# Optimization experiments

Measured on AMD Instinct MI355X. Metric: run time of the kernel, lower is better.

Reference implementation:

```python
import jax, jax.numpy as jnp
import numpy as np

V = 32000   # vocab_size
H = 256     # num_hiddens
B = 32      # batch
T = 128     # seq_len


def setup_inputs() -> dict:
    key = jax.random.key(0)
    ks = jax.random.split(key, 10)
    s = 0.05  # keep pre-activations in a sane range
    return {
        "X": jax.random.randint(ks[0], (B, T), 0, V),
        "H0": jnp.zeros((B, H), jnp.float32),
        "Wz": (jax.random.normal(ks[1], (H, V + H)) * s).astype(jnp.float32),
        "bz": (jax.random.normal(ks[2], (H,)) * s).astype(jnp.float32),
        "Wr": (jax.random.normal(ks[3], (H, V + H)) * s).astype(jnp.float32),
        "br": (jax.random.normal(ks[4], (H,)) * s).astype(jnp.float32),
        "Wh": (jax.random.normal(ks[5], (H, V + H)) * s).astype(jnp.float32),
        "bh": (jax.random.normal(ks[6], (H,)) * s).astype(jnp.float32),
        "Wo": (jax.random.normal(ks[7], (V, H)) * s).astype(jnp.float32),
        "bo": (jax.random.normal(ks[8], (V,)) * s).astype(jnp.float32),
    }


def reference(X, H0, Wz, bz, Wr, br, Wh, bh, Wo, bo):
    # nn.Linear(cat(one_hot(x), h)) == gather of the vocab-columns + h @ Wh.T.
    # one_hot(x) @ W[:, :V].T  ==  W[:, :V].T[x]  (row gather), same math, no dense one-hot GEMM.
    vocab = Wo.shape[0]
    Wz_x, Wz_h = Wz[:, :vocab], Wz[:, vocab:]
    Wr_x, Wr_h = Wr[:, :vocab], Wr[:, vocab:]
    Wh_x, Wh_h = Wh[:, :vocab], Wh[:, vocab:]

    Xt = X.T                 # [T, B] -- matches X.T in torch forward
    gz = Wz_x.T[Xt]          # [T, B, H]
    gr = Wr_x.T[Xt]          # [T, B, H]
    gh = Wh_x.T[Xt]          # [T, B, H]

    def step(Hs, g):
        gz_t, gr_t, gh_t = g
        z = jax.nn.sigmoid(gz_t + Hs @ Wz_h.T + bz)
        r = jax.nn.sigmoid(gr_t + Hs @ Wr_h.T + br)
        h = jnp.tanh(gh_t + (r * Hs) @ Wh_h.T + bh)
        Hn = z * h + (1.0 - z) * Hs
        Y = Hn @ Wo.T + bo   # [B, V]
        return Hn, Y

    Hf, Ys = jax.lax.scan(step, H0, (gz, gr, gh))  # Ys: [T, B, V]
    # torch.cat(outputs, dim=0) stacks time-major -> [T*B, V]
    return Ys.reshape(-1, vocab), Hf
```

## Files before the change

### kernel.cpp

```cpp
#include <hip/hip_runtime.h>
#include <hip/hip_fp16.h>
#include <stdint.h>

#define VV 32000
#define HH 256
#define BB 32
#define TT 128
#define VH 32256

typedef _Float16 f16;
typedef _Float16 f16x2 __attribute__((ext_vector_type(2)));
typedef _Float16 f16x8 __attribute__((ext_vector_type(8)));
typedef float f32x4 __attribute__((ext_vector_type(4)));

static __device__ __forceinline__ float dot2f(uint32_t w, uint32_t h, float acc){
  f16x2 a = __builtin_bit_cast(f16x2, w);
  f16x2 b = __builtin_bit_cast(f16x2, h);
#if __has_builtin(__builtin_amdgcn_fdot2)
  return __builtin_amdgcn_fdot2(a, b, acc, false);
#else
  acc = fmaf((float)a[0], (float)b[0], acc);
  acc = fmaf((float)a[1], (float)b[1], acc);
  return acc;
#endif
}

__global__ void k_gather(const int* __restrict__ X,
                         const float* __restrict__ Wz, const float* __restrict__ bz,
                         const float* __restrict__ Wr, const float* __restrict__ br,
                         const float* __restrict__ Wh, const float* __restrict__ bh,
                         float* __restrict__ g_buf){
  int tb = blockIdx.x;
  int t = tb >> 5, b = tb & 31;
  int tok = X[b*TT + t];
  int o = threadIdx.x;
  g_buf[(size_t)tb*768 + o]       = Wz[(size_t)o*VH + tok] + bz[o];
  g_buf[(size_t)tb*768 + 256 + o] = Wr[(size_t)o*VH + tok] + br[o];
  g_buf[(size_t)tb*768 + 512 + o] = Wh[(size_t)o*VH + tok] + bh[o];
}

__global__ void k_pack(const float* __restrict__ Wz, const float* __restrict__ Wr,
                       const float* __restrict__ Wh, uint32_t* __restrict__ Wpack){
  int idx = blockIdx.x*256 + threadIdx.x;
  if (idx >= 512*192) return;
  int t = idx / 192, rem = idx - t*192;
  int ol = rem >> 4, p = rem & 15;
  int ko = t & 7, no = t >> 3;
  int k = ko*32 + p*2;
  const float* W; int row;
  if (ol < 8){ int o = no*8 + ol; if (o < 256){ W = Wz; row = o; } else { W = Wr; row = o - 256; } }
  else { W = Wh; row = no*4 + (ol - 8); }
  float a = W[(size_t)row*VH + VV + k];
  float c = W[(size_t)row*VH + VV + k + 1];
  f16x2 v; v[0] = (f16)a; v[1] = (f16)c;
  Wpack[idx] = __builtin_bit_cast(uint32_t, v);
}

__global__ __launch_bounds__(512)
__attribute__((amdgpu_waves_per_eu(2, 2)))
void k_recur(const float* __restrict__ H0,
             const uint32_t* __restrict__ Wpack,
             const float* __restrict__ g_buf,
             f16* __restrict__ Hn16,
             float* __restrict__ hf_out){
  __shared__ __align__(16) uint32_t hs16[128];
  __shared__ __align__(16) f16 rHs16[256];
  __shared__ float hs32[256];
  __shared__ float z_s[256];

  const int b = blockIdx.x;
  const int tid = threadIdx.x;
  const int ko = tid & 7, no = tid >> 3;

  uint32_t w[12][16];
  {
    const uint4* src = (const uint4*)(Wpack + (size_t)tid*192);
    #pragma unroll
    for (int j=0;j<48;j++){
      uint4 v = src[j];
      int f = j*4;
      w[(f+0)>>4][(f+0)&15] = v.x;
      w[(f+1)>>4][(f+1)&15] = v.y;
      w[(f+2)>>4][(f+2)&15] = v.z;
      w[(f+3)>>4][(f+3)&15] = v.w;
    }
  }

  if (tid < 256) hs32[tid] = H0[b*HH + tid];
  __syncthreads();
  if (tid < 128){
    f16x2 v; v[0] = (f16)hs32[2*tid]; v[1] = (f16)hs32[2*tid+1];
    hs16[tid] = __builtin_bit_cast(uint32_t, v);
  }
  __syncthreads();

  const int gi1 = no*8 + ko;
  const int gi2 = 512 + no*4 + (ko & 3);
  float g1 = g_buf[(size_t)b*768 + gi1];
  float g2 = g_buf[(size_t)b*768 + gi2];
  float g1n = 0.f, g2n = 0.f;

  for (int t = 0; t < TT; t++){
    if (t < TT-1){
      const float* gn = g_buf + (size_t)((t+1)*BB + b)*768;
      g1n = gn[gi1];
      g2n = gn[gi2];
    }

    uint32_t hp[16];
    {
      const uint2* hsp = (const uint2*)hs16;
      #pragma unroll
      for (int j=0;j<8;j++){ uint2 v = hsp[ko*8 + j]; hp[2*j] = v.x; hp[2*j+1] = v.y; }
    }
    float acc[8];
    #pragma unroll
    for (int ol=0;ol<8;ol++) acc[ol] = 0.f;
    #pragma unroll
    for (int p=0;p<16;p++)
      #pragma unroll
      for (int ol=0;ol<8;ol++)
        acc[ol] = dot2f(w[ol][p], hp[p], acc[ol]);
    #pragma unroll
    for (int ol=0;ol<8;ol++){
      float v2 = acc[ol];
      v2 += __shfl_xor(v2, 1);
      v2 += __shfl_xor(v2, 2);
      v2 += __shfl_xor(v2, 4);
      acc[ol] = v2;
    }
    {
      float sel = acc[0];
      #pragma unroll
      for (int ol=1;ol<8;ol++) sel = (ko == ol) ? acc[ol] : sel;
      float pre = sel + g1;
      float s = 1.f / (1.f + __expf(-pre));
      int o = no*8 + ko;
      if (no < 32){
        z_s[o] = s;
      } else {
        int op = o - 256;
        rHs16[op] = (f16)(s * hs32[op]);
      }
    }
    __syncthreads();

    uint32_t rp[16];
    {
      const uint2* rpp = (const uint2*)rHs16;
      #pragma unroll
      for (int j=0;j<8;j++){ uint2 v = rpp[ko*8 + j]; rp[2*j] = v.x; rp[2*j+1] = v.y; }
    }
    float a2[4];
    #pragma unroll
    for (int oi=0;oi<4;oi++) a2[oi] = 0.f;
    #pragma unroll
    for (int p=0;p<16;p++)
      #pragma unroll
      for (int oi=0;oi<4;oi++)
        a2[oi] = dot2f(w[8+oi][p], rp[p], a2[oi]);
    #pragma unroll
    for (int oi=0;oi<4;oi++){
      float v2 = a2[oi];
      v2 += __shfl_xor(v2, 1);
      v2 += __shfl_xor(v2, 2);
      v2 += __shfl_xor(v2, 4);
      a2[oi] = v2;
    }
    if (ko < 4){
      float sel = a2[0];
      #pragma unroll
      for (int oi=1;oi<4;oi++) sel = (ko == oi) ? a2[oi] : sel;
      int o = no*4 + ko;
      float pre = sel + g2;
      float ax = fabsf(pre);
      float e = __expf(2.f*ax);
      float th = 1.f - 2.f/(e + 1.f);
      th = copysignf(th, pre);
      float z = z_s[o];
      float hn = z*th + (1.f - z)*hs32[o];
      hs32[o] = hn;
      ((f16*)hs16)[o] = (f16)hn;
      Hn16[(size_t)(t*BB + b)*HH + o] = (f16)hn;
      if (t == TT-1) hf_out[b*HH + o] = hn;
    }
    g1 = g1n; g2 = g2n;
    __syncthreads();
  }
}

__global__ __launch_bounds__(256) void k_gemm(const f16* __restrict__ A, const float* __restrict__ Wo,
                                              const float* __restrict__ bo, float* __restrict__ Y){
  __shared__ __align__(16) f16 a_lds[128*128];
  __shared__ __align__(16) f16 b_lds[128*128];
  const int m0 = blockIdx.x * 128;
  const int n0 = blockIdx.y * 128;
  const int tid = threadIdx.x;
  const int lane = tid & 63, wave = tid >> 6;
  const int wm = wave >> 1, wn = wave & 1;

  f32x4 acc[4][4];
  {
    f32x4 z = {0.f, 0.f, 0.f, 0.f};
    #pragma unroll
    for (int i=0;i<4;i++)
      #pragma unroll
      for (int j=0;j<4;j++) acc[i][j] = z;
  }

  const int srow = tid >> 1, seg = tid & 1;
  #pragma unroll 1
  for (int kt=0; kt<2; kt++){
    const int k0 = kt*128;
    {
      const uint4* asrc = (const uint4*)(A + (size_t)(m0+srow)*256 + k0 + seg*64);
      #pragma unroll
      for (int j=0;j<8;j++){
        uint4 v = asrc[j];
        int byte = (srow*256 + seg*128 + j*16) ^ ((srow&7)<<4);
        *(uint4*)((char*)a_lds + byte) = v;
      }
      const float4* bsrc = (const float4*)(Wo + (size_t)(n0+srow)*256 + k0 + seg*64);
      #pragma unroll
      for (int j=0;j<8;j++){
        float4 f0 = bsrc[2*j], f1 = bsrc[2*j+1];
        f16x8 hv;
        hv[0]=(f16)f0.x; hv[1]=(f16)f0.y; hv[2]=(f16)f0.z; hv[3]=(f16)f0.w;
        hv[4]=(f16)f1.x; hv[5]=(f16)f1.y; hv[6]=(f16)f1.z; hv[7]=(f16)f1.w;
        int byte = (srow*256 + seg*128 + j*16) ^ ((srow&7)<<4);
        *(f16x8*)((char*)b_lds + byte) = hv;
      }
    }
    __syncthreads();
    #pragma unroll
    for (int kk=0; kk<4; kk++){
      const int kbyte = kk*64 + (lane>>4)*16;
      f16x8 af[4], bf[4];
      #pragma unroll
      for (int mi=0;mi<4;mi++){
        int row = wm*64 + mi*16 + (lane&15);
        int byte = (row*256 + kbyte) ^ ((row&7)<<4);
        af[mi] = *(const f16x8*)((const char*)a_lds + byte);
      }
      #pragma unroll
      for (int nj=0;nj<4;nj++){
        int nl = wn*64 + nj*16 + (lane&15);
        int byte = (nl*256 + kbyte) ^ ((nl&7)<<4);
        bf[nj] = *(const f16x8*)((const char*)b_lds + byte);
      }
      #pragma unroll
      for (int mi=0;mi<4;mi++)
        #pragma unroll
        for (int nj=0;nj<4;nj++)
          acc[mi][nj] = __builtin_amdgcn_mfma_f32_16x16x32_f16(af[mi], bf[nj], acc[mi][nj], 0, 0, 0);
    }
    __syncthreads();
  }
  #pragma unroll
  for (int nj=0;nj<4;nj++){
    const int col = n0 + wn*64 + nj*16 + (lane & 15);
    const float bov = bo[col];
    #pragma unroll
    for (int mi=0;mi<4;mi++){
      const int rbase = m0 + wm*64 + mi*16 + (lane>>4)*4;
      #pragma unroll
      for (int r=0;r<4;r++){
        Y[(size_t)(rbase + r)*VV + col] = acc[mi][nj][r] + bov;
      }
    }
  }
}

extern "C" void kernel_launch(void* const* d_in, const int* in_sizes, int n_in,
                              void* d_out, int out_size, void* d_ws, size_t ws_size,
                              hipStream_t stream){
  const int*   X  = (const int*)d_in[0];
  const float* H0 = (const float*)d_in[1];
  const float* Wz = (const float*)d_in[2];
  const float* bz = (const float*)d_in[3];
  const float* Wr = (const float*)d_in[4];
  const float* br = (const float*)d_in[5];
  const float* Wh = (const float*)d_in[6];
  const float* bh = (const float*)d_in[7];
  const float* Wo = (const float*)d_in[8];
  const float* bo = (const float*)d_in[9];
  float* out = (float*)d_out;

  char* ws = (char*)d_ws;
  float*    g_buf = (float*)ws;
  uint32_t* Wpack = (uint32_t*)(ws + 12582912);
  f16*      Hn16  = (f16*)(ws + 12582912 + 393216);

  k_gather<<<4096, 256, 0, stream>>>(X, Wz, bz, Wr, br, Wh, bh, g_buf);
  k_pack<<<384, 256, 0, stream>>>(Wz, Wr, Wh, Wpack);
  k_recur<<<32, 512, 0, stream>>>(H0, Wpack, g_buf, Hn16, out + 131072000LL);
  k_gemm<<<dim3(32, 250), 256, 0, stream>>>(Hn16, Wo, bo, out);
}
```

Before: 549.3 us.

## Pre-convert Wo to fp16, pin recurrent weights in AGPRs, remap GEMM tiles

After: 689.7 us. 1.26x slower.

```diff
diff --git a/kernel.cpp b/kernel.cpp
--- a/kernel.cpp
+++ b/kernel.cpp
@@ -56,6 +56,37 @@
   Wpack[idx] = __builtin_bit_cast(uint32_t, v);
 }
 
+__global__ void k_wo(const float* __restrict__ Wo, f16* __restrict__ Wof){
+  int i = blockIdx.x*256 + threadIdx.x;
+  const float4* s = (const float4*)Wo + (size_t)i*2;
+  float4 f0 = s[0], f1 = s[1];
+  f16x8 h;
+  h[0]=(f16)f0.x; h[1]=(f16)f0.y; h[2]=(f16)f0.z; h[3]=(f16)f0.w;
+  h[4]=(f16)f1.x; h[5]=(f16)f1.y; h[6]=(f16)f1.z; h[7]=(f16)f1.w;
+  *(f16x8*)(Wof + (size_t)i*8) = h;
+}
+
+#define DECL16(P) uint32_t P##_0,P##_1,P##_2,P##_3,P##_4,P##_5,P##_6,P##_7, \
+                           P##_8,P##_9,P##_10,P##_11,P##_12,P##_13,P##_14,P##_15;
+#define LDQ(j,e0,e1,e2,e3) { uint4 v_ = src[j]; \
+  asm("v_accvgpr_write_b32 %0, %1" : "=a"(e0) : "v"(v_.x)); \
+  asm("v_accvgpr_write_b32 %0, %1" : "=a"(e1) : "v"(v_.y)); \
+  asm("v_accvgpr_write_b32 %0, %1" : "=a"(e2) : "v"(v_.z)); \
+  asm("v_accvgpr_write_b32 %0, %1" : "=a"(e3) : "v"(v_.w)); }
+#define LDROW(r,P) LDQ(4*(r)+0,P##_0,P##_1,P##_2,P##_3)   LDQ(4*(r)+1,P##_4,P##_5,P##_6,P##_7) \
+                   LDQ(4*(r)+2,P##_8,P##_9,P##_10,P##_11) LDQ(4*(r)+3,P##_12,P##_13,P##_14,P##_15)
+#define RD(a_) __extension__({ uint32_t t_; \
+  asm volatile("v_accvgpr_read_b32 %0, %1" : "=v"(t_) : "a"(a_)); t_; })
+#define DOTP1(p) \
+  a0 = dot2f(RD(w0_##p), hp[p], a0);  a1 = dot2f(RD(w1_##p), hp[p], a1); \
+  a2 = dot2f(RD(w2_##p), hp[p], a2);  a3 = dot2f(RD(w3_##p), hp[p], a3); \
+  a4 = dot2f(RD(w4_##p), hp[p], a4);  a5 = dot2f(RD(w5_##p), hp[p], a5); \
+  a6 = dot2f(RD(w6_##p), hp[p], a6);  a7 = dot2f(RD(w7_##p), hp[p], a7);
+#define DOTP2(p) \
+  b0 = dot2f(RD(w8_##p),  rp[p], b0); b1 = dot2f(RD(w9_##p),  rp[p], b1); \
+  b2 = dot2f(RD(w10_##p), rp[p], b2); b3 = dot2f(RD(w11_##p), rp[p], b3);
+#define REDUCE(x) x += __shfl_xor(x,1); x += __shfl_xor(x,2); x += __shfl_xor(x,4);
+
 __global__ __launch_bounds__(512)
 __attribute__((amdgpu_waves_per_eu(2, 2)))
 void k_recur(const float* __restrict__ H0,
@@ -72,18 +103,12 @@
   const int tid = threadIdx.x;
   const int ko = tid & 7, no = tid >> 3;
 
-  uint32_t w[12][16];
+  DECL16(w0) DECL16(w1) DECL16(w2)  DECL16(w3)  DECL16(w4)  DECL16(w5)
+  DECL16(w6) DECL16(w7) DECL16(w8)  DECL16(w9)  DECL16(w10) DECL16(w11)
   {
     const uint4* src = (const uint4*)(Wpack + (size_t)tid*192);
-    #pragma unroll
-    for (int j=0;j<48;j++){
-      uint4 v = src[j];
-      int f = j*4;
-      w[(f+0)>>4][(f+0)&15] = v.x;
-      w[(f+1)>>4][(f+1)&15] = v.y;
-      w[(f+2)>>4][(f+2)&15] = v.z;
-      w[(f+3)>>4][(f+3)&15] = v.w;
-    }
+    LDROW(0,w0) LDROW(1,w1) LDROW(2,w2)   LDROW(3,w3)  LDROW(4,w4)  LDROW(5,w5)
+    LDROW(6,w6) LDROW(7,w7) LDROW(8,w8)   LDROW(9,w9)  LDROW(10,w10) LDROW(11,w11)
   }
 
   if (tid < 256) hs32[tid] = H0[b*HH + tid];
@@ -113,26 +138,14 @@
       #pragma unroll
       for (int j=0;j<8;j++){ uint2 v = hsp[ko*8 + j]; hp[2*j] = v.x; hp[2*j+1] = v.y; }
     }
-    float acc[8];
-    #pragma unroll
-    for (int ol=0;ol<8;ol++) acc[ol] = 0.f;
-    #pragma unroll
-    for (int p=0;p<16;p++)
-      #pragma unroll
-      for (int ol=0;ol<8;ol++)
-        acc[ol] = dot2f(w[ol][p], hp[p], acc[ol]);
-    #pragma unroll
-    for (int ol=0;ol<8;ol++){
-      float v2 = acc[ol];
-      v2 += __shfl_xor(v2, 1);
-      v2 += __shfl_xor(v2, 2);
-      v2 += __shfl_xor(v2, 4);
-      acc[ol] = v2;
-    }
-    {
-      float sel = acc[0];
-      #pragma unroll
-      for (int ol=1;ol<8;ol++) sel = (ko == ol) ? acc[ol] : sel;
+    float a0=0.f,a1=0.f,a2=0.f,a3=0.f,a4=0.f,a5=0.f,a6=0.f,a7=0.f;
+    DOTP1(0)  DOTP1(1)  DOTP1(2)  DOTP1(3)  DOTP1(4)  DOTP1(5)  DOTP1(6)  DOTP1(7)
+    DOTP1(8)  DOTP1(9)  DOTP1(10) DOTP1(11) DOTP1(12) DOTP1(13) DOTP1(14) DOTP1(15)
+    REDUCE(a0) REDUCE(a1) REDUCE(a2) REDUCE(a3) REDUCE(a4) REDUCE(a5) REDUCE(a6) REDUCE(a7)
+    {
+      float sel = a0;
+      sel = (ko==1)?a1:sel; sel = (ko==2)?a2:sel; sel = (ko==3)?a3:sel;
+      sel = (ko==4)?a4:sel; sel = (ko==5)?a5:sel; sel = (ko==6)?a6:sel; sel = (ko==7)?a7:sel;
       float pre = sel + g1;
       float s = 1.f / (1.f + __expf(-pre));
       int o = no*8 + ko;
@@ -151,26 +164,13 @@
       #pragma unroll
       for (int j=0;j<8;j++){ uint2 v = rpp[ko*8 + j]; rp[2*j] = v.x; rp[2*j+1] = v.y; }
     }
-    float a2[4];
-    #pragma unroll
-    for (int oi=0;oi<4;oi++) a2[oi] = 0.f;
-    #pragma unroll
-    for (int p=0;p<16;p++)
-      #pragma unroll
-      for (int oi=0;oi<4;oi++)
-        a2[oi] = dot2f(w[8+oi][p], rp[p], a2[oi]);
-    #pragma unroll
-    for (int oi=0;oi<4;oi++){
-      float v2 = a2[oi];
-      v2 += __shfl_xor(v2, 1);
-      v2 += __shfl_xor(v2, 2);
-      v2 += __shfl_xor(v2, 4);
-      a2[oi] = v2;
-    }
+    float b0=0.f,b1=0.f,b2=0.f,b3=0.f;
+    DOTP2(0)  DOTP2(1)  DOTP2(2)  DOTP2(3)  DOTP2(4)  DOTP2(5)  DOTP2(6)  DOTP2(7)
+    DOTP2(8)  DOTP2(9)  DOTP2(10) DOTP2(11) DOTP2(12) DOTP2(13) DOTP2(14) DOTP2(15)
+    REDUCE(b0) REDUCE(b1) REDUCE(b2) REDUCE(b3)
     if (ko < 4){
-      float sel = a2[0];
-      #pragma unroll
-      for (int oi=1;oi<4;oi++) sel = (ko == oi) ? a2[oi] : sel;
+      float sel = b0;
+      sel = (ko==1)?b1:sel; sel = (ko==2)?b2:sel; sel = (ko==3)?b3:sel;
       int o = no*4 + ko;
       float pre = sel + g2;
       float ax = fabsf(pre);
@@ -189,12 +189,13 @@
   }
 }
 
-__global__ __launch_bounds__(256) void k_gemm(const f16* __restrict__ A, const float* __restrict__ Wo,
+__global__ __launch_bounds__(256) void k_gemm(const f16* __restrict__ A, const f16* __restrict__ Wof,
                                               const float* __restrict__ bo, float* __restrict__ Y){
   __shared__ __align__(16) f16 a_lds[128*128];
   __shared__ __align__(16) f16 b_lds[128*128];
-  const int m0 = blockIdx.x * 128;
-  const int n0 = blockIdx.y * 128;
+  const int wg = (blockIdx.x & 7)*1000 + (blockIdx.x >> 3);
+  const int m0 = (wg & 31) * 128;
+  const int n0 = (wg >> 5) * 128;
   const int tid = threadIdx.x;
   const int lane = tid & 63, wave = tid >> 6;
   const int wm = wave >> 1, wn = wave & 1;
@@ -214,21 +215,14 @@
     const int k0 = kt*128;
     {
       const uint4* asrc = (const uint4*)(A + (size_t)(m0+srow)*256 + k0 + seg*64);
+      const uint4* bsrc = (const uint4*)(Wof + (size_t)(n0+srow)*256 + k0 + seg*64);
       #pragma unroll
       for (int j=0;j<8;j++){
-        uint4 v = asrc[j];
+        uint4 av = asrc[j];
         int byte = (srow*256 + seg*128 + j*16) ^ ((srow&7)<<4);
-        *(uint4*)((char*)a_lds + byte) = v;
-      }
-      const float4* bsrc = (const float4*)(Wo + (size_t)(n0+srow)*256 + k0 + seg*64);
-      #pragma unroll
-      for (int j=0;j<8;j++){
-        float4 f0 = bsrc[2*j], f1 = bsrc[2*j+1];
-        f16x8 hv;
-        hv[0]=(f16)f0.x; hv[1]=(f16)f0.y; hv[2]=(f16)f0.z; hv[3]=(f16)f0.w;
-        hv[4]=(f16)f1.x; hv[5]=(f16)f1.y; hv[6]=(f16)f1.z; hv[7]=(f16)f1.w;
-        int byte = (srow*256 + seg*128 + j*16) ^ ((srow&7)<<4);
-        *(f16x8*)((char*)b_lds + byte) = hv;
+        *(uint4*)((char*)a_lds + byte) = av;
+        uint4 bv = bsrc[j];
+        *(uint4*)((char*)b_lds + byte) = bv;
       }
     }
     __syncthreads();
@@ -290,9 +284,11 @@
   float*    g_buf = (float*)ws;
   uint32_t* Wpack = (uint32_t*)(ws + 12582912);
   f16*      Hn16  = (f16*)(ws + 12582912 + 393216);
+  f16*      Wof   = (f16*)(ws + 12582912 + 393216 + 2097152);
 
   k_gather<<<4096, 256, 0, stream>>>(X, Wz, bz, Wr, br, Wh, bh, g_buf);
   k_pack<<<384, 256, 0, stream>>>(Wz, Wr, Wh, Wpack);
+  k_wo<<<4000, 256, 0, stream>>>(Wo, Wof);
   k_recur<<<32, 512, 0, stream>>>(H0, Wpack, g_buf, Hn16, out + 131072000LL);
-  k_gemm<<<dim3(32, 250), 256, 0, stream>>>(Hn16, Wo, bo, out);
-}
+  k_gemm<<<8000, 256, 0, stream>>>(Hn16, Wof, bo, out);
+}
```
